# Kernel tuning notes

Hardware: AMD Instinct MI355X
Metric: run time of the kernel (lower is better)

Reference implementation:

```python
import jax, jax.numpy as jnp
import numpy as np

MARGIN = 1.0  # from init_kwargs


def _cdist(a, b):
    # Euclidean pairwise distances, [N, D] x [M, D] -> [N, M]
    sq = (jnp.sum(a * a, axis=1)[:, None]
          + jnp.sum(b * b, axis=1)[None, :]
          - 2.0 * (a @ b.T))
    return jnp.sqrt(jnp.maximum(sq, 0.0))


def setup_inputs() -> dict:
    key = jax.random.key(0)
    k1, k2 = jax.random.split(key)
    N, D = 8192, 128
    return {
        "output1": jax.random.normal(k1, (N, D), dtype=jnp.float32),
        "output2": jax.random.normal(k2, (N, D), dtype=jnp.float32),
    }


def reference(output1, output2):
    d = _cdist(output1, output2)  # [N, M]
    N, M = d.shape

    # image -> text direction (loop over rows i in the original)
    jmin = jnp.argmin(d, axis=1)            # [N] positive index per row
    pos_r = jnp.min(d, axis=1)              # [N] pos_distance = d[i, jmin[i]]
    hinge_r = jnp.maximum(0.0, MARGIN - pos_r[:, None] + d)  # [N, M]
    # exclude the positive (argmin) column from each row's mean
    hinge_r = jnp.where(jnp.arange(M)[None, :] == jmin[:, None], 0.0, hinge_r)
    image_losses = hinge_r.mean(axis=1)     # [N]

    # text -> image direction (loop over columns i in the original)
    imin = jnp.argmin(d, axis=0)            # [M]
    pos_c = jnp.min(d, axis=0)              # [M]
    hinge_c = jnp.maximum(0.0, MARGIN - pos_c[None, :] + d)  # [N, M]
    hinge_c = jnp.where(jnp.arange(N)[:, None] == imin[None, :], 0.0, hinge_c)
    text_losses = hinge_c.mean(axis=0)      # [M]

    return (image_losses.mean() + text_losses.mean()) * 0.5
```

## Files before the change

### kernel.cpp

```cpp
#include <hip/hip_runtime.h>
#include <hip/hip_bf16.h>
#include <math.h>

#define NN 8192
#define DD 128
#define BIGF 3.402823466e+38f

typedef __attribute__((ext_vector_type(8))) short short8;
typedef __attribute__((ext_vector_type(4))) float f32x4;

static __device__ __forceinline__ unsigned short bfc(float f) {
    return __bfloat16_as_ushort(__float2bfloat16(f));
}

__global__ __launch_bounds__(256) void prep_kernel(const float* __restrict__ A,
                                                   const float* __restrict__ B,
                                                   __hip_bfloat16* __restrict__ Abf,
                                                   __hip_bfloat16* __restrict__ Bbf,
                                                   float* __restrict__ na,
                                                   float* __restrict__ nb,
                                                   unsigned int* __restrict__ done) {
    if (blockIdx.y == 0 && blockIdx.x == 0 && threadIdx.x == 0) *done = 0u;
    const float* x = blockIdx.y ? B : A;
    __hip_bfloat16* xb = blockIdx.y ? Bbf : Abf;
    float* norm = blockIdx.y ? nb : na;
    const int sub = threadIdx.x >> 5;
    const int ch  = threadIdx.x & 31;
    const int row = blockIdx.x * 8 + sub;
    const float4 v = *(const float4*)(x + (size_t)row * DD + ch * 4);
    float s = v.x * v.x + v.y * v.y + v.z * v.z + v.w * v.w;
    uint2 pk;
    pk.x = ((unsigned)bfc(v.y) << 16) | bfc(v.x);
    pk.y = ((unsigned)bfc(v.w) << 16) | bfc(v.z);
    *(uint2*)(xb + (size_t)row * DD + ch * 4) = pk;
#pragma unroll
    for (int off = 16; off >= 1; off >>= 1) s += __shfl_xor(s, off, 64);
    if (ch == 0) norm[row] = s;
}

__global__ __launch_bounds__(256, 4) void dist_fused(
    const __hip_bfloat16* __restrict__ Ab, const __hip_bfloat16* __restrict__ Bb,
    const float* __restrict__ na, const float* __restrict__ nb,
    float* __restrict__ rowpart, float* __restrict__ colpart,
    float* __restrict__ totpart) {
    __shared__ char lds[32768];
    __shared__ float rmbuf[2][128];
    __shared__ float cmbuf[2][128];
    __shared__ float tbuf[4];
    char* ldsA = lds;
    char* ldsB = lds + 16384;
    const int tid = threadIdx.x;

    const int lin = blockIdx.y * 64 + blockIdx.x;
    const int swz = (lin & 7) * 512 + (lin >> 3);
    const int bx = swz & 63, by = swz >> 6;
    const int rowBase = by * 128;
    const int colBase = bx * 128;

    const unsigned short* aG = (const unsigned short*)Ab + (size_t)rowBase * DD;
    const unsigned short* bG = (const unsigned short*)Bb + (size_t)colBase * DD;

    const int l = tid & 63, wid = tid >> 6;
    const int wr = wid >> 1, wc = wid & 1;
    const int g = l >> 4, c = l & 15;

    f32x4 acc[4][4];
#pragma unroll
    for (int mi = 0; mi < 4; ++mi)
#pragma unroll
        for (int ni = 0; ni < 4; ++ni) acc[mi][ni] = (f32x4)0.f;

#pragma unroll
    for (int p = 0; p < 2; ++p) {
        if (p) __syncthreads();
#pragma unroll
        for (int it = 0; it < 4; ++it) {
            int idx = tid + 256 * it;
            int r = idx >> 3;
            int c16 = idx & 7;
            int dst = r * 128 + ((c16 * 16) ^ ((r & 7) << 4));
            *(short8*)(ldsA + dst) = *(const short8*)(aG + r * DD + p * 64 + c16 * 8);
            *(short8*)(ldsB + dst) = *(const short8*)(bG + r * DD + p * 64 + c16 * 8);
        }
        __syncthreads();
#pragma unroll
        for (int kk = 0; kk < 2; ++kk) {
            short8 af[4], bf[4];
            const int kbyte = kk * 64 + g * 16;
#pragma unroll
            for (int mi = 0; mi < 4; ++mi) {
                int r = wr * 64 + mi * 16 + c;
                af[mi] = *(const short8*)(ldsA + r * 128 + (kbyte ^ ((r & 7) << 4)));
                int r2 = wc * 64 + mi * 16 + c;
                bf[mi] = *(const short8*)(ldsB + r2 * 128 + (kbyte ^ ((r2 & 7) << 4)));
            }
#pragma unroll
            for (int mi = 0; mi < 4; ++mi)
#pragma unroll
                for (int ni = 0; ni < 4; ++ni)
                    acc[mi][ni] = __builtin_amdgcn_mfma_f32_16x16x32_bf16(
                        af[mi], bf[ni], acc[mi][ni], 0, 0, 0);
        }
    }

    const int row0 = rowBase + wr * 64;
    const int col0 = colBase + wc * 64;

    float nbc[4];
#pragma unroll
    for (int ni = 0; ni < 4; ++ni) nbc[ni] = nb[col0 + ni * 16 + c];

    float colm2[4] = {BIGF, BIGF, BIGF, BIGF};
    f32x4 tot4 = (f32x4)0.f;
#pragma unroll
    for (int mi = 0; mi < 4; ++mi) {
        const f32x4 na4 = *(const f32x4*)(na + row0 + mi * 16 + g * 4);
        float rowm2[4] = {BIGF, BIGF, BIGF, BIGF};
#pragma unroll
        for (int ni = 0; ni < 4; ++ni) {
            f32x4 a = acc[mi][ni];
#pragma unroll
            for (int reg = 0; reg < 4; ++reg) {
                float d2 = fmaf(-2.0f, a[reg], na4[reg] + nbc[ni]);
                rowm2[reg] = fminf(rowm2[reg], d2);
                colm2[ni] = fminf(colm2[ni], d2);
                tot4[reg] += __builtin_amdgcn_sqrtf(fmaxf(d2, 0.f));
            }
        }
#pragma unroll
        for (int reg = 0; reg < 4; ++reg) {
            float m = rowm2[reg];
            m = fminf(m, __shfl_xor(m, 1, 64));
            m = fminf(m, __shfl_xor(m, 2, 64));
            m = fminf(m, __shfl_xor(m, 4, 64));
            m = fminf(m, __shfl_xor(m, 8, 64));
            if (c == 0) rmbuf[wc][wr * 64 + mi * 16 + g * 4 + reg] = m;
        }
    }
#pragma unroll
    for (int ni = 0; ni < 4; ++ni) {
        float m = colm2[ni];
        m = fminf(m, __shfl_xor(m, 16, 64));
        m = fminf(m, __shfl_xor(m, 32, 64));
        if (g == 0) cmbuf[wr][wc * 64 + ni * 16 + c] = m;
    }
    float tot = (tot4[0] + tot4[1]) + (tot4[2] + tot4[3]);
#pragma unroll
    for (int off = 32; off >= 1; off >>= 1) tot += __shfl_xor(tot, off, 64);
    if (l == 0) tbuf[wid] = tot;
    __syncthreads();

    if (tid < 128) {
        rowpart[(size_t)bx * NN + rowBase + tid] = fminf(rmbuf[0][tid], rmbuf[1][tid]);
    } else if (tid < 256) {
        int j = tid - 128;
        colpart[(size_t)by * NN + colBase + j] = fminf(cmbuf[0][j], cmbuf[1][j]);
    }
    if (tid == 0)
        totpart[by * 64 + bx] = tbuf[0] + tbuf[1] + tbuf[2] + tbuf[3];
}

__global__ __launch_bounds__(256) void fin_kernel(const float* __restrict__ rowpart,
                                                  const float* __restrict__ colpart,
                                                  const float* __restrict__ totpart,
                                                  float* __restrict__ finpart,
                                                  unsigned int* __restrict__ done,
                                                  float* __restrict__ out) {
    const int idx = blockIdx.x * 256 + threadIdx.x;
    const int j = (idx < NN) ? idx : idx - NN;
    const float* p = (idx < NN) ? rowpart : colpart;
    float m = BIGF;
#pragma unroll 8
    for (int k = 0; k < 64; ++k) m = fminf(m, p[(size_t)k * NN + j]);
    float contrib = -__builtin_amdgcn_sqrtf(fmaxf(m, 0.f)) * (1.0f / 16384.0f);
    if (blockIdx.x < 16)
        contrib += totpart[blockIdx.x * 256 + threadIdx.x] * (1.0f / 67108864.0f);
#pragma unroll
    for (int off = 32; off >= 1; off >>= 1) contrib += __shfl_xor(contrib, off, 64);
    __shared__ float red[4];
    __shared__ unsigned last;
    if ((threadIdx.x & 63) == 0) red[threadIdx.x >> 6] = contrib;
    __syncthreads();
    if (threadIdx.x == 0) {
        finpart[blockIdx.x] = red[0] + red[1] + red[2] + red[3];
        __threadfence();
        last = (atomicAdd(done, 1u) == 63u) ? 1u : 0u;
    }
    __syncthreads();
    if (last && threadIdx.x < 64) {
        __threadfence();
        float s = __hip_atomic_load(&finpart[threadIdx.x], __ATOMIC_RELAXED,
                                    __HIP_MEMORY_SCOPE_AGENT);
#pragma unroll
        for (int off = 32; off >= 1; off >>= 1) s += __shfl_xor(s, off, 64);
        if (threadIdx.x == 0) out[0] = s + 1.0f - 1.0f / 8192.0f;
    }
}

extern "C" void kernel_launch(void* const* d_in, const int* in_sizes, int n_in,
                              void* d_out, int out_size, void* d_ws, size_t ws_size,
                              hipStream_t stream) {
    const float* A = (const float*)d_in[0];
    const float* B = (const float*)d_in[1];
    char* ws = (char*)d_ws;

    const size_t MB = 1024 * 1024;
    __hip_bfloat16* Abf = (__hip_bfloat16*)(ws);
    __hip_bfloat16* Bbf = (__hip_bfloat16*)(ws + 2 * MB);
    float* na      = (float*)(ws + 4 * MB);
    float* nb      = (float*)(ws + 4 * MB + 32768);
    float* rowpart = (float*)(ws + 4 * MB + 65536);
    float* colpart = (float*)(ws + 6 * MB + 65536);
    float* totpart = (float*)(ws + 8 * MB + 65536);
    float* finpart = (float*)(ws + 8 * MB + 65536 + 16384);
    unsigned int* done = (unsigned int*)(ws + 8 * MB + 65536 + 16384 + 256);

    dim3 pgrid(NN / 8, 2);
    prep_kernel<<<pgrid, 256, 0, stream>>>(A, B, Abf, Bbf, na, nb, done);

    dim3 grid(NN / 128, NN / 128);
    dist_fused<<<grid, 256, 0, stream>>>(Abf, Bbf, na, nb, rowpart, colpart, totpart);

    fin_kernel<<<64, 256, 0, stream>>>(rowpart, colpart, totpart, finpart, done,
                                       (float*)d_out);
}
```

Baseline: 66.72 us.

## Fuse bf16 conversion and row norms into the distance kernel, drop prep pass

Removes the separate prep kernel that converted inputs to bf16 and computed squared norms. Each distance tile now loads fp32 inputs directly, computes the squared norms via shuffles into shared memory, and packs to bf16 while staging into LDS. This saves a launch and an intermediate buffer round trip. In exchange it doubles the global load bytes per tile and repeats conversion work across tiles, and lowers the occupancy hint from 4 to 3 blocks.

Result: slower. 162.0 us (+142.9%).

```diff
diff --git a/kernel.cpp b/kernel.cpp
--- a/kernel.cpp
+++ b/kernel.cpp
@@ -12,38 +12,24 @@
 static __device__ __forceinline__ unsigned short bfc(float f) {
     return __bfloat16_as_ushort(__float2bfloat16(f));
 }
-
-__global__ __launch_bounds__(256) void prep_kernel(const float* __restrict__ A,
-                                                   const float* __restrict__ B,
-                                                   __hip_bfloat16* __restrict__ Abf,
-                                                   __hip_bfloat16* __restrict__ Bbf,
-                                                   float* __restrict__ na,
-                                                   float* __restrict__ nb,
-                                                   unsigned int* __restrict__ done) {
-    if (blockIdx.y == 0 && blockIdx.x == 0 && threadIdx.x == 0) *done = 0u;
-    const float* x = blockIdx.y ? B : A;
-    __hip_bfloat16* xb = blockIdx.y ? Bbf : Abf;
-    float* norm = blockIdx.y ? nb : na;
-    const int sub = threadIdx.x >> 5;
-    const int ch  = threadIdx.x & 31;
-    const int row = blockIdx.x * 8 + sub;
-    const float4 v = *(const float4*)(x + (size_t)row * DD + ch * 4);
-    float s = v.x * v.x + v.y * v.y + v.z * v.z + v.w * v.w;
-    uint2 pk;
-    pk.x = ((unsigned)bfc(v.y) << 16) | bfc(v.x);
-    pk.y = ((unsigned)bfc(v.w) << 16) | bfc(v.z);
-    *(uint2*)(xb + (size_t)row * DD + ch * 4) = pk;
-#pragma unroll
-    for (int off = 16; off >= 1; off >>= 1) s += __shfl_xor(s, off, 64);
-    if (ch == 0) norm[row] = s;
-}
-
-__global__ __launch_bounds__(256, 4) void dist_fused(
-    const __hip_bfloat16* __restrict__ Ab, const __hip_bfloat16* __restrict__ Bb,
-    const float* __restrict__ na, const float* __restrict__ nb,
+static __device__ __forceinline__ short8 pk8(float4 a, float4 b) {
+    short8 s;
+    s[0] = (short)bfc(a.x); s[1] = (short)bfc(a.y);
+    s[2] = (short)bfc(a.z); s[3] = (short)bfc(a.w);
+    s[4] = (short)bfc(b.x); s[5] = (short)bfc(b.y);
+    s[6] = (short)bfc(b.z); s[7] = (short)bfc(b.w);
+    return s;
+}
+static __device__ __forceinline__ float sq4(float4 v) {
+    return v.x * v.x + v.y * v.y + v.z * v.z + v.w * v.w;
+}
+
+__global__ __launch_bounds__(256, 3) void dist_fused(
+    const float* __restrict__ A32, const float* __restrict__ B32,
     float* __restrict__ rowpart, float* __restrict__ colpart,
-    float* __restrict__ totpart) {
+    float* __restrict__ totpart, unsigned int* __restrict__ done) {
     __shared__ char lds[32768];
+    __shared__ float nrmA[128], nrmB[128];
     __shared__ float rmbuf[2][128];
     __shared__ float cmbuf[2][128];
     __shared__ float tbuf[4];
@@ -51,14 +37,16 @@
     char* ldsB = lds + 16384;
     const int tid = threadIdx.x;
 
+    if (blockIdx.x == 0 && blockIdx.y == 0 && tid == 0) *done = 0u;
+
     const int lin = blockIdx.y * 64 + blockIdx.x;
     const int swz = (lin & 7) * 512 + (lin >> 3);
     const int bx = swz & 63, by = swz >> 6;
     const int rowBase = by * 128;
     const int colBase = bx * 128;
 
-    const unsigned short* aG = (const unsigned short*)Ab + (size_t)rowBase * DD;
-    const unsigned short* bG = (const unsigned short*)Bb + (size_t)colBase * DD;
+    const float* aG = A32 + (size_t)rowBase * DD;
+    const float* bG = B32 + (size_t)colBase * DD;
 
     const int l = tid & 63, wid = tid >> 6;
     const int wr = wid >> 1, wc = wid & 1;
@@ -69,6 +57,9 @@
     for (int mi = 0; mi < 4; ++mi)
 #pragma unroll
         for (int ni = 0; ni < 4; ++ni) acc[mi][ni] = (f32x4)0.f;
+
+    float ssA[4] = {0.f, 0.f, 0.f, 0.f};
+    float ssB[4] = {0.f, 0.f, 0.f, 0.f};
 
 #pragma unroll
     for (int p = 0; p < 2; ++p) {
@@ -78,9 +69,30 @@
             int idx = tid + 256 * it;
             int r = idx >> 3;
             int c16 = idx & 7;
+            const float* pa = aG + r * DD + p * 64 + c16 * 8;
+            const float* pb = bG + r * DD + p * 64 + c16 * 8;
+            float4 va0 = *(const float4*)pa, va1 = *(const float4*)(pa + 4);
+            float4 vb0 = *(const float4*)pb, vb1 = *(const float4*)(pb + 4);
+            ssA[it] += sq4(va0) + sq4(va1);
+            ssB[it] += sq4(vb0) + sq4(vb1);
             int dst = r * 128 + ((c16 * 16) ^ ((r & 7) << 4));
-            *(short8*)(ldsA + dst) = *(const short8*)(aG + r * DD + p * 64 + c16 * 8);
-            *(short8*)(ldsB + dst) = *(const short8*)(bG + r * DD + p * 64 + c16 * 8);
+            *(short8*)(ldsA + dst) = pk8(va0, va1);
+            *(short8*)(ldsB + dst) = pk8(vb0, vb1);
+        }
+        if (p == 1) {
+#pragma unroll
+            for (int it = 0; it < 4; ++it) {
+                int r = (tid + 256 * it) >> 3;
+                float sa = ssA[it];
+                sa += __shfl_xor(sa, 1, 64);
+                sa += __shfl_xor(sa, 2, 64);
+                sa += __shfl_xor(sa, 4, 64);
+                float sb = ssB[it];
+                sb += __shfl_xor(sb, 1, 64);
+                sb += __shfl_xor(sb, 2, 64);
+                sb += __shfl_xor(sb, 4, 64);
+                if ((tid & 7) == 0) { nrmA[r] = sa; nrmB[r] = sb; }
+            }
         }
         __syncthreads();
 #pragma unroll
@@ -108,13 +120,13 @@
 
     float nbc[4];
 #pragma unroll
-    for (int ni = 0; ni < 4; ++ni) nbc[ni] = nb[col0 + ni * 16 + c];
+    for (int ni = 0; ni < 4; ++ni) nbc[ni] = nrmB[wc * 64 + ni * 16 + c];
 
     float colm2[4] = {BIGF, BIGF, BIGF, BIGF};
     f32x4 tot4 = (f32x4)0.f;
 #pragma unroll
     for (int mi = 0; mi < 4; ++mi) {
-        const f32x4 na4 = *(const f32x4*)(na + row0 + mi * 16 + g * 4);
+        const f32x4 na4 = *(const f32x4*)&nrmA[wr * 64 + mi * 16 + g * 4];
         float rowm2[4] = {BIGF, BIGF, BIGF, BIGF};
 #pragma unroll
         for (int ni = 0; ni < 4; ++ni) {
@@ -205,21 +217,14 @@
     char* ws = (char*)d_ws;
 
     const size_t MB = 1024 * 1024;
-    __hip_bfloat16* Abf = (__hip_bfloat16*)(ws);
-    __hip_bfloat16* Bbf = (__hip_bfloat16*)(ws + 2 * MB);
-    float* na      = (float*)(ws + 4 * MB);
-    float* nb      = (float*)(ws + 4 * MB + 32768);
-    float* rowpart = (float*)(ws + 4 * MB + 65536);
-    float* colpart = (float*)(ws + 6 * MB + 65536);
-    float* totpart = (float*)(ws + 8 * MB + 65536);
-    float* finpart = (float*)(ws + 8 * MB + 65536 + 16384);
-    unsigned int* done = (unsigned int*)(ws + 8 * MB + 65536 + 16384 + 256);
-
-    dim3 pgrid(NN / 8, 2);
-    prep_kernel<<<pgrid, 256, 0, stream>>>(A, B, Abf, Bbf, na, nb, done);
+    float* rowpart = (float*)(ws);
+    float* colpart = (float*)(ws + 2 * MB);
+    float* totpart = (float*)(ws + 4 * MB);
+    float* finpart = (float*)(ws + 4 * MB + 16384);
+    unsigned int* done = (unsigned int*)(ws + 4 * MB + 16384 + 256);
 
     dim3 grid(NN / 128, NN / 128);
-    dist_fused<<<grid, 256, 0, stream>>>(Abf, Bbf, na, nb, rowpart, colpart, totpart);
+    dist_fused<<<grid, 256, 0, stream>>>(A, B, rowpart, colpart, totpart, done);
 
     fin_kernel<<<64, 256, 0, stream>>>(rowpart, colpart, totpart, finpart, done,
                                        (float*)d_out);
```

## Use 256x128 tiles with 512 threads and register-prefetch the second K half

Applied to the files above, without the earlier changes.

The distance kernel now processes 256-row by 128-column tiles with 8 waves per block, halving the grid and the number of column partial-min rows. Global loads for the second half of K are issued into registers before the first compute phase, so they overlap with the first MFMA phase. The finalize kernel and workspace layout are adjusted for 32 column partials and 2048 tile totals. The larger tile and prefetch registers raise LDS and register use, which may cut occupancy.

Result: no change. 67.69 us (+1.5%).

```diff
diff --git a/kernel.cpp b/kernel.cpp
--- a/kernel.cpp
+++ b/kernel.cpp
@@ -38,70 +38,105 @@
     if (ch == 0) norm[row] = s;
 }
 
-__global__ __launch_bounds__(256, 4) void dist_fused(
+__global__ __launch_bounds__(512, 4) void dist_fused(
     const __hip_bfloat16* __restrict__ Ab, const __hip_bfloat16* __restrict__ Bb,
     const float* __restrict__ na, const float* __restrict__ nb,
     float* __restrict__ rowpart, float* __restrict__ colpart,
     float* __restrict__ totpart) {
-    __shared__ char lds[32768];
-    __shared__ float rmbuf[2][128];
-    __shared__ float cmbuf[2][128];
-    __shared__ float tbuf[4];
+    __shared__ char lds[49152];
+    __shared__ float rmbuf[2][256];
+    __shared__ float cmbuf[4][128];
+    __shared__ float tbuf[8];
     char* ldsA = lds;
-    char* ldsB = lds + 16384;
+    char* ldsB = lds + 32768;
     const int tid = threadIdx.x;
-
-    const int lin = blockIdx.y * 64 + blockIdx.x;
-    const int swz = (lin & 7) * 512 + (lin >> 3);
-    const int bx = swz & 63, by = swz >> 6;
-    const int rowBase = by * 128;
-    const int colBase = bx * 128;
-
-    const unsigned short* aG = (const unsigned short*)Ab + (size_t)rowBase * DD;
-    const unsigned short* bG = (const unsigned short*)Bb + (size_t)colBase * DD;
-
     const int l = tid & 63, wid = tid >> 6;
     const int wr = wid >> 1, wc = wid & 1;
     const int g = l >> 4, c = l & 15;
 
+    const int lin = blockIdx.y * 64 + blockIdx.x;
+    const int swz = (lin & 7) * 256 + (lin >> 3);
+    const int bx = swz & 63, by = swz >> 6;
+    const int rowBase = by * 256;
+    const int colBase = bx * 128;
+
+    const unsigned short* aG = (const unsigned short*)Ab + (size_t)rowBase * DD;
+    const unsigned short* bG = (const unsigned short*)Bb + (size_t)colBase * DD;
+
     f32x4 acc[4][4];
 #pragma unroll
     for (int mi = 0; mi < 4; ++mi)
 #pragma unroll
         for (int ni = 0; ni < 4; ++ni) acc[mi][ni] = (f32x4)0.f;
 
-#pragma unroll
-    for (int p = 0; p < 2; ++p) {
-        if (p) __syncthreads();
-#pragma unroll
-        for (int it = 0; it < 4; ++it) {
-            int idx = tid + 256 * it;
-            int r = idx >> 3;
-            int c16 = idx & 7;
-            int dst = r * 128 + ((c16 * 16) ^ ((r & 7) << 4));
-            *(short8*)(ldsA + dst) = *(const short8*)(aG + r * DD + p * 64 + c16 * 8);
-            *(short8*)(ldsB + dst) = *(const short8*)(bG + r * DD + p * 64 + c16 * 8);
-        }
-        __syncthreads();
-#pragma unroll
-        for (int kk = 0; kk < 2; ++kk) {
-            short8 af[4], bf[4];
-            const int kbyte = kk * 64 + g * 16;
-#pragma unroll
-            for (int mi = 0; mi < 4; ++mi) {
-                int r = wr * 64 + mi * 16 + c;
-                af[mi] = *(const short8*)(ldsA + r * 128 + (kbyte ^ ((r & 7) << 4)));
-                int r2 = wc * 64 + mi * 16 + c;
-                bf[mi] = *(const short8*)(ldsB + r2 * 128 + (kbyte ^ ((r2 & 7) << 4)));
-            }
-#pragma unroll
-            for (int mi = 0; mi < 4; ++mi)
-#pragma unroll
-                for (int ni = 0; ni < 4; ++ni)
-                    acc[mi][ni] = __builtin_amdgcn_mfma_f32_16x16x32_bf16(
-                        af[mi], bf[ni], acc[mi][ni], 0, 0, 0);
-        }
-    }
+    short8 sa[4], sb[2], ta[4], tb[2];
+#pragma unroll
+    for (int it = 0; it < 4; ++it) {
+        int idx = tid + 512 * it;
+        sa[it] = *(const short8*)(aG + (idx >> 3) * DD + (idx & 7) * 8);
+    }
+#pragma unroll
+    for (int it = 0; it < 2; ++it) {
+        int idx = tid + 512 * it;
+        sb[it] = *(const short8*)(bG + (idx >> 3) * DD + (idx & 7) * 8);
+    }
+#pragma unroll
+    for (int it = 0; it < 4; ++it) {
+        int idx = tid + 512 * it, r = idx >> 3, c16 = idx & 7;
+        *(short8*)(ldsA + r * 128 + ((c16 * 16) ^ ((r & 7) << 4))) = sa[it];
+    }
+#pragma unroll
+    for (int it = 0; it < 2; ++it) {
+        int idx = tid + 512 * it, r = idx >> 3, c16 = idx & 7;
+        *(short8*)(ldsB + r * 128 + ((c16 * 16) ^ ((r & 7) << 4))) = sb[it];
+    }
+#pragma unroll
+    for (int it = 0; it < 4; ++it) {
+        int idx = tid + 512 * it;
+        ta[it] = *(const short8*)(aG + (idx >> 3) * DD + 64 + (idx & 7) * 8);
+    }
+#pragma unroll
+    for (int it = 0; it < 2; ++it) {
+        int idx = tid + 512 * it;
+        tb[it] = *(const short8*)(bG + (idx >> 3) * DD + 64 + (idx & 7) * 8);
+    }
+    __syncthreads();
+
+#define COMPUTE_PHASE() do {                                                      \
+    _Pragma("unroll")                                                             \
+    for (int kk = 0; kk < 2; ++kk) {                                              \
+        short8 af[4], bf[4];                                                      \
+        const int kbyte = kk * 64 + g * 16;                                       \
+        _Pragma("unroll")                                                         \
+        for (int mi = 0; mi < 4; ++mi) {                                          \
+            int r = wr * 64 + mi * 16 + c;                                        \
+            af[mi] = *(const short8*)(ldsA + r * 128 + (kbyte ^ ((r & 7) << 4))); \
+            int r2 = wc * 64 + mi * 16 + c;                                       \
+            bf[mi] = *(const short8*)(ldsB + r2 * 128 + (kbyte ^ ((r2 & 7) << 4)));\
+        }                                                                         \
+        _Pragma("unroll")                                                         \
+        for (int mi = 0; mi < 4; ++mi)                                            \
+            _Pragma("unroll")                                                     \
+            for (int ni = 0; ni < 4; ++ni)                                        \
+                acc[mi][ni] = __builtin_amdgcn_mfma_f32_16x16x32_bf16(            \
+                    af[mi], bf[ni], acc[mi][ni], 0, 0, 0);                        \
+    } } while (0)
+
+    COMPUTE_PHASE();
+    __syncthreads();
+#pragma unroll
+    for (int it = 0; it < 4; ++it) {
+        int idx = tid + 512 * it, r = idx >> 3, c16 = idx & 7;
+        *(short8*)(ldsA + r * 128 + ((c16 * 16) ^ ((r & 7) << 4))) = ta[it];
+    }
+#pragma unroll
+    for (int it = 0; it < 2; ++it) {
+        int idx = tid + 512 * it, r = idx >> 3, c16 = idx & 7;
+        *(short8*)(ldsB + r * 128 + ((c16 * 16) ^ ((r & 7) << 4))) = tb[it];
+    }
+    __syncthreads();
+    COMPUTE_PHASE();
+#undef COMPUTE_PHASE
 
     const int row0 = rowBase + wr * 64;
     const int col0 = colBase + wc * 64;
@@ -150,14 +185,18 @@
     if (l == 0) tbuf[wid] = tot;
     __syncthreads();
 
-    if (tid < 128) {
+    if (tid < 256) {
         rowpart[(size_t)bx * NN + rowBase + tid] = fminf(rmbuf[0][tid], rmbuf[1][tid]);
-    } else if (tid < 256) {
-        int j = tid - 128;
-        colpart[(size_t)by * NN + colBase + j] = fminf(cmbuf[0][j], cmbuf[1][j]);
-    }
-    if (tid == 0)
-        totpart[by * 64 + bx] = tbuf[0] + tbuf[1] + tbuf[2] + tbuf[3];
+    } else if (tid < 384) {
+        int j = tid - 256;
+        colpart[(size_t)by * NN + colBase + j] =
+            fminf(fminf(cmbuf[0][j], cmbuf[1][j]), fminf(cmbuf[2][j], cmbuf[3][j]));
+    } else if (tid == 384) {
+        float s = 0.f;
+#pragma unroll
+        for (int w = 0; w < 8; ++w) s += tbuf[w];
+        totpart[by * 64 + bx] = s;
+    }
 }
 
 __global__ __launch_bounds__(256) void fin_kernel(const float* __restrict__ rowpart,
@@ -167,13 +206,17 @@
                                                   unsigned int* __restrict__ done,
                                                   float* __restrict__ out) {
     const int idx = blockIdx.x * 256 + threadIdx.x;
-    const int j = (idx < NN) ? idx : idx - NN;
-    const float* p = (idx < NN) ? rowpart : colpart;
     float m = BIGF;
+    if (idx < NN) {
 #pragma unroll 8
-    for (int k = 0; k < 64; ++k) m = fminf(m, p[(size_t)k * NN + j]);
+        for (int k = 0; k < 64; ++k) m = fminf(m, rowpart[(size_t)k * NN + idx]);
+    } else {
+        const int j = idx - NN;
+#pragma unroll 8
+        for (int k = 0; k < 32; ++k) m = fminf(m, colpart[(size_t)k * NN + j]);
+    }
     float contrib = -__builtin_amdgcn_sqrtf(fmaxf(m, 0.f)) * (1.0f / 16384.0f);
-    if (blockIdx.x < 16)
+    if (blockIdx.x < 8)
         contrib += totpart[blockIdx.x * 256 + threadIdx.x] * (1.0f / 67108864.0f);
 #pragma unroll
     for (int off = 32; off >= 1; off >>= 1) contrib += __shfl_xor(contrib, off, 64);
@@ -211,15 +254,15 @@
     float* nb      = (float*)(ws + 4 * MB + 32768);
     float* rowpart = (float*)(ws + 4 * MB + 65536);
     float* colpart = (float*)(ws + 6 * MB + 65536);
-    float* totpart = (float*)(ws + 8 * MB + 65536);
-    float* finpart = (float*)(ws + 8 * MB + 65536 + 16384);
-    unsigned int* done = (unsigned int*)(ws + 8 * MB + 65536 + 16384 + 256);
+    float* totpart = (float*)(ws + 7 * MB + 65536);
+    float* finpart = (float*)(ws + 7 * MB + 65536 + 8192);
+    unsigned int* done = (unsigned int*)(ws + 7 * MB + 65536 + 8192 + 256);
 
     dim3 pgrid(NN / 8, 2);
     prep_kernel<<<pgrid, 256, 0, stream>>>(A, B, Abf, Bbf, na, nb, done);
 
-    dim3 grid(NN / 128, NN / 128);
-    dist_fused<<<grid, 256, 0, stream>>>(Abf, Bbf, na, nb, rowpart, colpart, totpart);
+    dim3 grid(64, 32);
+    dist_fused<<<grid, 512, 0, stream>>>(Abf, Bbf, na, nb, rowpart, colpart, totpart);
 
     fin_kernel<<<64, 256, 0, stream>>>(rowpart, colpart, totpart, finpart, done,
                                        (float*)d_out);
```

## Merge prep, distance and finalize into one persistent cooperative kernel

Applied to the files above, without the earlier changes.

Replaces the three kernel launches with a single persistent cooperative kernel. Blocks loop over the prep rows, the 4096 distance tiles and the final reduction, with grid-wide syncs between phases and an atomicAdd into the output. The aim is to remove launch gaps and tail effects between kernels. The cost is two grid barriers, possible lower occupancy or imbalance in the tile loop, a host occupancy query on every call, and a fallback multi-kernel path if the cooperative launch fails.

After: 228.7 us. 3.43x slower.

```diff
diff --git a/kernel.cpp b/kernel.cpp
--- a/kernel.cpp
+++ b/kernel.cpp
@@ -1,4 +1,5 @@
 #include <hip/hip_runtime.h>
+#include <hip/hip_cooperative_groups.h>
 #include <hip/hip_bf16.h>
 #include <math.h>
 
@@ -6,6 +7,8 @@
 #define DD 128
 #define BIGF 3.402823466e+38f
 
+namespace cg = cooperative_groups;
+
 typedef __attribute__((ext_vector_type(8))) short short8;
 typedef __attribute__((ext_vector_type(4))) float f32x4;
 
@@ -13,20 +16,13 @@
     return __bfloat16_as_ushort(__float2bfloat16(f));
 }
 
-__global__ __launch_bounds__(256) void prep_kernel(const float* __restrict__ A,
-                                                   const float* __restrict__ B,
-                                                   __hip_bfloat16* __restrict__ Abf,
-                                                   __hip_bfloat16* __restrict__ Bbf,
-                                                   float* __restrict__ na,
-                                                   float* __restrict__ nb,
-                                                   unsigned int* __restrict__ done) {
-    if (blockIdx.y == 0 && blockIdx.x == 0 && threadIdx.x == 0) *done = 0u;
-    const float* x = blockIdx.y ? B : A;
-    __hip_bfloat16* xb = blockIdx.y ? Bbf : Abf;
-    float* norm = blockIdx.y ? nb : na;
-    const int sub = threadIdx.x >> 5;
-    const int ch  = threadIdx.x & 31;
-    const int row = blockIdx.x * 8 + sub;
+
+static __device__ __forceinline__ void prep_unit(const float* __restrict__ x,
+                                                 __hip_bfloat16* __restrict__ xb,
+                                                 float* __restrict__ nrm,
+                                                 int oct, int tid) {
+    const int sub = tid >> 5, ch = tid & 31;
+    const int row = oct * 8 + sub;
     const float4 v = *(const float4*)(x + (size_t)row * DD + ch * 4);
     float s = v.x * v.x + v.y * v.y + v.z * v.z + v.w * v.w;
     uint2 pk;
@@ -35,31 +31,22 @@
     *(uint2*)(xb + (size_t)row * DD + ch * 4) = pk;
 #pragma unroll
     for (int off = 16; off >= 1; off >>= 1) s += __shfl_xor(s, off, 64);
-    if (ch == 0) norm[row] = s;
-}
-
-__global__ __launch_bounds__(256, 4) void dist_fused(
+    if (ch == 0) nrm[row] = s;
+}
+
+static __device__ __forceinline__ void dist_tile(
+    int bx, int by, char* lds, float (*rmbuf)[128], float (*cmbuf)[128],
+    float* tbuf,
     const __hip_bfloat16* __restrict__ Ab, const __hip_bfloat16* __restrict__ Bb,
-    const float* __restrict__ na, const float* __restrict__ nb,
+    const float* __restrict__ nA, const float* __restrict__ nB,
     float* __restrict__ rowpart, float* __restrict__ colpart,
-    float* __restrict__ totpart) {
-    __shared__ char lds[32768];
-    __shared__ float rmbuf[2][128];
-    __shared__ float cmbuf[2][128];
-    __shared__ float tbuf[4];
+    float* __restrict__ totpart, int tid) {
     char* ldsA = lds;
     char* ldsB = lds + 16384;
-    const int tid = threadIdx.x;
-
-    const int lin = blockIdx.y * 64 + blockIdx.x;
-    const int swz = (lin & 7) * 512 + (lin >> 3);
-    const int bx = swz & 63, by = swz >> 6;
     const int rowBase = by * 128;
     const int colBase = bx * 128;
-
     const unsigned short* aG = (const unsigned short*)Ab + (size_t)rowBase * DD;
     const unsigned short* bG = (const unsigned short*)Bb + (size_t)colBase * DD;
-
     const int l = tid & 63, wid = tid >> 6;
     const int wr = wid >> 1, wc = wid & 1;
     const int g = l >> 4, c = l & 15;
@@ -105,16 +92,15 @@
 
     const int row0 = rowBase + wr * 64;
     const int col0 = colBase + wc * 64;
-
     float nbc[4];
 #pragma unroll
-    for (int ni = 0; ni < 4; ++ni) nbc[ni] = nb[col0 + ni * 16 + c];
+    for (int ni = 0; ni < 4; ++ni) nbc[ni] = nB[col0 + ni * 16 + c];
 
     float colm2[4] = {BIGF, BIGF, BIGF, BIGF};
     f32x4 tot4 = (f32x4)0.f;
 #pragma unroll
     for (int mi = 0; mi < 4; ++mi) {
-        const f32x4 na4 = *(const f32x4*)(na + row0 + mi * 16 + g * 4);
+        const f32x4 na4 = *(const f32x4*)(nA + row0 + mi * 16 + g * 4);
         float rowm2[4] = {BIGF, BIGF, BIGF, BIGF};
 #pragma unroll
         for (int ni = 0; ni < 4; ++ni) {
@@ -160,12 +146,85 @@
         totpart[by * 64 + bx] = tbuf[0] + tbuf[1] + tbuf[2] + tbuf[3];
 }
 
-__global__ __launch_bounds__(256) void fin_kernel(const float* __restrict__ rowpart,
-                                                  const float* __restrict__ colpart,
-                                                  const float* __restrict__ totpart,
-                                                  float* __restrict__ finpart,
-                                                  unsigned int* __restrict__ done,
-                                                  float* __restrict__ out) {
+__global__ __launch_bounds__(256, 4) void mono_kernel(
+    const float* __restrict__ A32, const float* __restrict__ B32,
+    __hip_bfloat16* __restrict__ Abf, __hip_bfloat16* __restrict__ Bbf,
+    float* __restrict__ nA, float* __restrict__ nB,
+    float* __restrict__ rowpart, float* __restrict__ colpart,
+    float* __restrict__ totpart, float* __restrict__ out, int NBK) {
+    __shared__ char lds[32768];
+    __shared__ float rmbuf[2][128];
+    __shared__ float cmbuf[2][128];
+    __shared__ float tbuf[4];
+    cg::grid_group grid = cg::this_grid();
+    const int bid = blockIdx.x;
+    const int tid = threadIdx.x;
+
+    for (int u = bid; u < 2048; u += NBK) {
+        const int mat = u >> 10, oct = u & 1023;
+        prep_unit(mat ? B32 : A32, mat ? Bbf : Abf, mat ? nB : nA, oct, tid);
+    }
+    if (bid == 0 && tid == 0) out[0] = 1.0f - 1.0f / 8192.0f;
+    grid.sync();
+
+    for (int t = bid; t < 4096; t += NBK) {
+        const int swz = (t & 7) * 512 + (t >> 3);
+        dist_tile(swz & 63, swz >> 6, lds, rmbuf, cmbuf, tbuf,
+                  Abf, Bbf, nA, nB, rowpart, colpart, totpart, tid);
+        __syncthreads();
+    }
+    grid.sync();
+
+    for (int u = bid; u < 64; u += NBK) {
+        const int idx = u * 256 + tid;
+        const int j = (idx < NN) ? idx : idx - NN;
+        const float* p = (idx < NN) ? rowpart : colpart;
+        float m = BIGF;
+#pragma unroll 8
+        for (int k = 0; k < 64; ++k) m = fminf(m, p[(size_t)k * NN + j]);
+        float contrib = -__builtin_amdgcn_sqrtf(fmaxf(m, 0.f)) * (1.0f / 16384.0f);
+        if (u < 16) contrib += totpart[u * 256 + tid] * (1.0f / 67108864.0f);
+#pragma unroll
+        for (int off = 32; off >= 1; off >>= 1) contrib += __shfl_xor(contrib, off, 64);
+        if ((tid & 63) == 0) tbuf[tid >> 6] = contrib;
+        __syncthreads();
+        if (tid == 0) atomicAdd(out, tbuf[0] + tbuf[1] + tbuf[2] + tbuf[3]);
+        __syncthreads();
+    }
+}
+
+__global__ __launch_bounds__(256) void prep_kernel(const float* __restrict__ A,
+                                                   const float* __restrict__ B,
+                                                   __hip_bfloat16* __restrict__ Abf,
+                                                   __hip_bfloat16* __restrict__ Bbf,
+                                                   float* __restrict__ nA,
+                                                   float* __restrict__ nB,
+                                                   float* __restrict__ out) {
+    if (blockIdx.x == 0 && blockIdx.y == 0 && threadIdx.x == 0)
+        out[0] = 1.0f - 1.0f / 8192.0f;
+    prep_unit(blockIdx.y ? B : A, blockIdx.y ? Bbf : Abf, blockIdx.y ? nB : nA,
+              blockIdx.x, threadIdx.x);
+}
+
+__global__ __launch_bounds__(256, 4) void dist_kernel(
+    const __hip_bfloat16* __restrict__ Ab, const __hip_bfloat16* __restrict__ Bb,
+    const float* __restrict__ nA, const float* __restrict__ nB,
+    float* __restrict__ rowpart, float* __restrict__ colpart,
+    float* __restrict__ totpart) {
+    __shared__ char lds[32768];
+    __shared__ float rmbuf[2][128];
+    __shared__ float cmbuf[2][128];
+    __shared__ float tbuf[4];
+    const int lin = blockIdx.y * 64 + blockIdx.x;
+    const int swz = (lin & 7) * 512 + (lin >> 3);
+    dist_tile(swz & 63, swz >> 6, lds, rmbuf, cmbuf, tbuf,
+              Ab, Bb, nA, nB, rowpart, colpart, totpart, threadIdx.x);
+}
+
+__global__ __launch_bounds__(256) void fin1_kernel(const float* __restrict__ rowpart,
+                                                   const float* __restrict__ colpart,
+                                                   const float* __restrict__ totpart,
+                                                   float* __restrict__ finpart) {
     const int idx = blockIdx.x * 256 + threadIdx.x;
     const int j = (idx < NN) ? idx : idx - NN;
     const float* p = (idx < NN) ? rowpart : colpart;
@@ -178,23 +237,18 @@
 #pragma unroll
     for (int off = 32; off >= 1; off >>= 1) contrib += __shfl_xor(contrib, off, 64);
     __shared__ float red[4];
-    __shared__ unsigned last;
     if ((threadIdx.x & 63) == 0) red[threadIdx.x >> 6] = contrib;
     __syncthreads();
-    if (threadIdx.x == 0) {
+    if (threadIdx.x == 0)
         finpart[blockIdx.x] = red[0] + red[1] + red[2] + red[3];
-        __threadfence();
-        last = (atomicAdd(done, 1u) == 63u) ? 1u : 0u;
-    }
-    __syncthreads();
-    if (last && threadIdx.x < 64) {
-        __threadfence();
-        float s = __hip_atomic_load(&finpart[threadIdx.x], __ATOMIC_RELAXED,
-                                    __HIP_MEMORY_SCOPE_AGENT);
-#pragma unroll
-        for (int off = 32; off >= 1; off >>= 1) s += __shfl_xor(s, off, 64);
-        if (threadIdx.x == 0) out[0] = s + 1.0f - 1.0f / 8192.0f;
-    }
+}
+
+__global__ __launch_bounds__(64) void fin2_kernel(const float* __restrict__ finpart,
+                                                  float* __restrict__ out) {
+    float s = finpart[threadIdx.x];
+#pragma unroll
+    for (int off = 32; off >= 1; off >>= 1) s += __shfl_xor(s, off, 64);
+    if (threadIdx.x == 0) out[0] += s;
 }
 
 extern "C" void kernel_launch(void* const* d_in, const int* in_sizes, int n_in,
@@ -207,20 +261,34 @@
     const size_t MB = 1024 * 1024;
     __hip_bfloat16* Abf = (__hip_bfloat16*)(ws);
     __hip_bfloat16* Bbf = (__hip_bfloat16*)(ws + 2 * MB);
-    float* na      = (float*)(ws + 4 * MB);
-    float* nb      = (float*)(ws + 4 * MB + 32768);
+    float* nA      = (float*)(ws + 4 * MB);
+    float* nB      = (float*)(ws + 4 * MB + 32768);
     float* rowpart = (float*)(ws + 4 * MB + 65536);
     float* colpart = (float*)(ws + 6 * MB + 65536);
     float* totpart = (float*)(ws + 8 * MB + 65536);
     float* finpart = (float*)(ws + 8 * MB + 65536 + 16384);
-    unsigned int* done = (unsigned int*)(ws + 8 * MB + 65536 + 16384 + 256);
-
-    dim3 pgrid(NN / 8, 2);
-    prep_kernel<<<pgrid, 256, 0, stream>>>(A, B, Abf, Bbf, na, nb, done);
-
-    dim3 grid(NN / 128, NN / 128);
-    dist_fused<<<grid, 256, 0, stream>>>(Abf, Bbf, na, nb, rowpart, colpart, totpart);
-
-    fin_kernel<<<64, 256, 0, stream>>>(rowpart, colpart, totpart, finpart, done,
-                                       (float*)d_out);
-}
+    float* outp    = (float*)d_out;
+
+    int maxb = 0;
+    (void)hipOccupancyMaxActiveBlocksPerMultiprocessor(&maxb, mono_kernel, 256, 0);
+    int nbk = (maxb > 0) ? maxb * 256 : 512;
+    if (nbk > 1024) nbk = 1024;
+    nbk &= ~7;
+    if (nbk < 64) nbk = 64;
+
+    void* args[] = {(void*)&A, (void*)&B, (void*)&Abf, (void*)&Bbf,
+                    (void*)&nA, (void*)&nB, (void*)&rowpart, (void*)&colpart,
+                    (void*)&totpart, (void*)&outp, (void*)&nbk};
+    hipError_t e = hipLaunchCooperativeKernel((void*)mono_kernel, dim3(nbk),
+                                              dim3(256), args, 0, stream);
+    if (e != hipSuccess) {
+        (void)hipGetLastError();
+        dim3 pgrid(NN / 8, 2);
+        prep_kernel<<<pgrid, 256, 0, stream>>>(A, B, Abf, Bbf, nA, nB, outp);
+        dim3 grid(NN / 128, NN / 128);
+        dist_kernel<<<grid, 256, 0, stream>>>(Abf, Bbf, nA, nB, rowpart, colpart,
+                                              totpart);
+        fin1_kernel<<<64, 256, 0, stream>>>(rowpart, colpart, totpart, finpart);
+        fin2_kernel<<<1, 64, 0, stream>>>(finpart, outp);
+    }
+}
```
